# Performance work log

Measured on AMD Instinct MI355X. Metric: run time of the kernel, lower is better.

## Reference

```python
import jax, jax.numpy as jnp
import numpy as np

N_HEADS = 8
HEAD_DIM = 64  # d_model // n_heads = 512 // 8


def setup_inputs() -> dict:
    key = jax.random.key(0)
    kq, kk, kv, km = jax.random.split(key, 4)
    B, C, H, L, D = 8, 4, N_HEADS, 512, HEAD_DIM
    q = jax.random.normal(kq, (B * C, H, L, D), dtype=jnp.float32)
    k = jax.random.normal(kk, (B * C, H, D, L), dtype=jnp.float32)  # pre-transposed, matmul(q, k) directly
    v = jax.random.normal(kv, (B * C, H, L, D), dtype=jnp.float32)
    attn_mask = jax.random.randint(km, (B, L, L), 0, 2).astype(bool)  # True = masked out
    return {"q": q, "k": k, "v": v, "attn_mask": attn_mask}


def reference(q, k, v, attn_mask):
    # q: [B*C, H, L, D]; k: [B*C, H, D, L]; v: [B*C, H, L, D]; attn_mask: [B, L, L] bool
    scale = jnp.asarray(HEAD_DIM ** (-0.5), dtype=q.dtype)
    scores = jnp.einsum('ghld,ghdm->ghlm', q, k) * scale  # [B*C, H, L, L]
    if attn_mask is not None:
        B = attn_mask.shape[0]
        C = q.shape[0] // B
        H, L = scores.shape[1], scores.shape[2]
        scores = scores.reshape(B, C, H, L, L)
        mask = attn_mask[:, None, None, :, :]  # broadcast over channels and heads
        scores = jnp.where(mask, -jnp.inf, scores)
        scores = scores.reshape(B * C, H, L, L)
    attn_weights = jax.nn.softmax(scores, axis=-1)  # dropout p=0.0 -> identity (eval)
    output = jnp.einsum('ghlm,ghmd->ghld', attn_weights, v)  # [B*C, H, L, D]
    return output
```

## Files before the change

kernel.cpp:

```cpp
#include <hip/hip_runtime.h>


typedef __attribute__((ext_vector_type(8)))  short bf16x8;
typedef __attribute__((ext_vector_type(16))) float f32x16;

union Frag4 { uint4 x; unsigned u[4]; bf16x8 v; };

__device__ __forceinline__ unsigned pk_bf16(float a, float b){
    unsigned ua = __builtin_bit_cast(unsigned, a) + 0x8000u;
    unsigned ub = __builtin_bit_cast(unsigned, b) + 0x8000u;
    return __builtin_amdgcn_perm(ub, ua, 0x07060302u);
}

__device__ __forceinline__ float fast_exp2(float x){
#if __has_builtin(__builtin_amdgcn_exp2f)
    return __builtin_amdgcn_exp2f(x);
#else
    return exp2f(x);
#endif
}

#define L2E 1.44269504088896f

__global__ __launch_bounds__(256, 4)
void attn_fused(const float* __restrict__ qg, const float* __restrict__ kg,
                const float* __restrict__ vg, const int* __restrict__ mg,
                float* __restrict__ og)
{
    __shared__ uint4 sKt4[64*8];
    __shared__ uint4 sVt4[64*8];

    const int t    = threadIdx.x;
    const int lane = t & 63;
    const int wv   = t >> 6;
    const int col  = lane & 31;
    const int h    = lane >> 5;

    const int bi   = blockIdx.x;
    const int s    = bi >> 3;
    const int head = (bi & 7)*32 + (s >> 2);
    const int qt   = s & 3;
    const int b    = bi & 7;

    const float* qh = qg + (size_t)head*32768;
    const float* kh = kg + (size_t)head*32768;
    const float* vh = vg + (size_t)head*32768;
    const int*   mb = mg + (size_t)b*262144 + (size_t)qt*128*512;
    float*       oh = og + (size_t)head*32768;

    Frag4 qf[4];
    {
        const int qrow = qt*128 + wv*32 + col;
        const float* qr = qh + qrow*64 + h*8;
        #pragma unroll
        for (int kt=0; kt<4; ++kt){
            float4 x0 = *(const float4*)(qr + kt*16);
            float4 x1 = *(const float4*)(qr + kt*16 + 4);
            qf[kt].u[0] = pk_bf16(x0.x*0.125f, x0.y*0.125f);
            qf[kt].u[1] = pk_bf16(x0.z*0.125f, x0.w*0.125f);
            qf[kt].u[2] = pk_bf16(x1.x*0.125f, x1.y*0.125f);
            qf[kt].u[3] = pk_bf16(x1.z*0.125f, x1.w*0.125f);
        }
    }

    f32x16 o0, o1;
    #pragma unroll
    for (int i=0;i<16;++i){ o0[i]=0.f; o1[i]=0.f; }
    float lsum = 0.f;

    for (int kb=0; kb<8; ++kb){
        __syncthreads();
        #pragma unroll
        for (int gi=0; gi<2; ++gi){
            const int g = wv + gi*4;
            const float* kp = kh + (size_t)(g*8)*512 + kb*64 + lane;
            float kv[8];
            #pragma unroll
            for (int dd=0; dd<8; ++dd) kv[dd] = kp[(size_t)dd*512];
            Frag4 w;
            w.u[0]=pk_bf16(kv[0],kv[1]); w.u[1]=pk_bf16(kv[2],kv[3]);
            w.u[2]=pk_bf16(kv[4],kv[5]); w.u[3]=pk_bf16(kv[6],kv[7]);
            sKt4[lane*8 + (g ^ (lane&7))] = w.x;
        }
        #pragma unroll
        for (int gi=0; gi<2; ++gi){
            const int g = wv + gi*4;
            const float* vp = vh + (size_t)(kb*64 + g*8)*64 + lane;
            float vv[8];
            #pragma unroll
            for (int mm=0; mm<8; ++mm) vv[mm] = vp[(size_t)mm*64];
            Frag4 w;
            w.u[0]=pk_bf16(vv[0],vv[1]); w.u[1]=pk_bf16(vv[2],vv[3]);
            w.u[2]=pk_bf16(vv[4],vv[5]); w.u[3]=pk_bf16(vv[6],vv[7]);
            sVt4[lane*8 + (g ^ (lane&7))] = w.x;
        }
        __syncthreads();

        const int qrl = wv*32 + col;
        const int* mrow = mb + (size_t)qrl*512 + kb*64;
        #pragma unroll
        for (int mt=0; mt<2; ++mt){
            f32x16 sc;
            #pragma unroll
            for (int i=0;i<16;++i) sc[i]=0.f;
            #pragma unroll
            for (int kt=0; kt<4; ++kt){
                const int r = mt*32 + col;
                Frag4 a; a.x = sKt4[r*8 + ((kt*2+h) ^ (r&7))];
                sc = __builtin_amdgcn_mfma_f32_32x32x16_bf16(a.v, qf[kt].v, sc, 0, 0, 0);
            }
            float p[16];
            #pragma unroll
            for (int rg=0; rg<4; ++rg){
                int4 mm = *(const int4*)(mrow + mt*32 + rg*8 + h*4);
                float e0 = mm.x ? 0.f : fast_exp2(sc[4*rg+0]*L2E);
                float e1 = mm.y ? 0.f : fast_exp2(sc[4*rg+1]*L2E);
                float e2 = mm.z ? 0.f : fast_exp2(sc[4*rg+2]*L2E);
                float e3 = mm.w ? 0.f : fast_exp2(sc[4*rg+3]*L2E);
                p[4*rg+0]=e0; p[4*rg+1]=e1; p[4*rg+2]=e2; p[4*rg+3]=e3;
                lsum += (e0+e1)+(e2+e3);
            }
            unsigned pp[8];
            #pragma unroll
            for (int r2=0; r2<8; ++r2) pp[r2] = pk_bf16(p[2*r2], p[2*r2+1]);

            #pragma unroll
            for (int c=0; c<2; ++c){
                unsigned keep0 = h ? pp[4*c+2] : pp[4*c+0];
                unsigned keep1 = h ? pp[4*c+3] : pp[4*c+1];
                unsigned give0 = h ? pp[4*c+0] : pp[4*c+2];
                unsigned give1 = h ? pp[4*c+1] : pp[4*c+3];
                unsigned got0 = (unsigned)__shfl_xor((int)give0, 32, 64);
                unsigned got1 = (unsigned)__shfl_xor((int)give1, 32, 64);
                Frag4 pa;
                pa.u[0] = h ? got0  : keep0;
                pa.u[1] = h ? got1  : keep1;
                pa.u[2] = h ? keep0 : got0;
                pa.u[3] = h ? keep1 : got1;
                const int gm = mt*4 + c*2 + h;
                Frag4 b0; b0.x = sVt4[col*8      + (gm ^ (col&7))];
                o0 = __builtin_amdgcn_mfma_f32_32x32x16_bf16(pa.v, b0.v, o0, 0, 0, 0);
                Frag4 b1; b1.x = sVt4[(32+col)*8 + (gm ^ ((32+col)&7))];
                o1 = __builtin_amdgcn_mfma_f32_32x32x16_bf16(pa.v, b1.v, o1, 0, 0, 0);
            }
        }
    }

    lsum += __shfl_xor(lsum, 32, 64);
    const float inv = 1.0f / lsum;
    float* ob = oh + (size_t)(qt*128 + wv*32)*64;
    #pragma unroll
    for (int r=0; r<16; ++r){
        const int qq = (r&3) + 8*(r>>2) + 4*h;
        const float iv = __shfl(inv, qq, 64);
        ob[(size_t)qq*64 + col]      = o0[r]*iv;
        ob[(size_t)qq*64 + 32 + col] = o1[r]*iv;
    }
}

extern "C" void kernel_launch(void* const* d_in, const int* in_sizes, int n_in,
                              void* d_out, int out_size, void* d_ws, size_t ws_size,
                              hipStream_t stream) {
    (void)in_sizes; (void)n_in; (void)d_ws; (void)ws_size; (void)out_size;
    const float* q = (const float*)d_in[0];
    const float* k = (const float*)d_in[1];
    const float* v = (const float*)d_in[2];
    const int*   m = (const int*)d_in[3];
    attn_fused<<<dim3(1024), dim3(256), 0, stream>>>(q, k, v, m, (float*)d_out);
}
```

Baseline: 174.9 us.

## Double-buffer K/V tiles in LDS and pre-pack attention mask to bitmask

Adds double-buffered shared memory for the K and V tiles. The next tile's global loads are issued before the current tile's MFMAs, and one barrier per iteration replaces two, to hide load latency. Separately, a pre-pass kernel packs the int32 mask into 64-bit ballot words in workspace, so the attention kernel reads 8 bytes per row-block instead of 256 bytes of ints. This costs an extra launch, doubles LDS use, and holds more registers for the prefetched values, which could reduce occupancy.

```diff
diff --git a/kernel.cpp b/kernel.cpp
--- a/kernel.cpp
+++ b/kernel.cpp
@@ -22,13 +22,29 @@
 
 #define L2E 1.44269504088896f
 
+__global__ __launch_bounds__(256)
+void pack_mask(const int* __restrict__ mg, unsigned long long* __restrict__ bits)
+{
+    const int t    = blockIdx.x*256 + threadIdx.x;
+    const int lane = t & 63;
+    const int w0   = t >> 6;
+    const int strd = (int)((gridDim.x*256) >> 6);
+    const int nW   = 8*512*8;
+    for (int i = w0; i < nW; i += strd){
+        int v = mg[(size_t)i*64 + lane];
+        unsigned long long m = __ballot(v != 0);
+        if (lane == 0) bits[i] = m;
+    }
+}
+
+template<int BITS>
 __global__ __launch_bounds__(256, 4)
 void attn_fused(const float* __restrict__ qg, const float* __restrict__ kg,
                 const float* __restrict__ vg, const int* __restrict__ mg,
-                float* __restrict__ og)
+                const unsigned* __restrict__ bits, float* __restrict__ og)
 {
-    __shared__ uint4 sKt4[64*8];
-    __shared__ uint4 sVt4[64*8];
+    __shared__ uint4 sKt4[2][64*8];
+    __shared__ uint4 sVt4[2][64*8];
 
     const int t    = threadIdx.x;
     const int lane = t & 63;
@@ -45,13 +61,18 @@
     const float* qh = qg + (size_t)head*32768;
     const float* kh = kg + (size_t)head*32768;
     const float* vh = vg + (size_t)head*32768;
-    const int*   mb = mg + (size_t)b*262144 + (size_t)qt*128*512;
     float*       oh = og + (size_t)head*32768;
+
+    const int qrl = wv*32 + col;
+    const int* mrow0 = BITS ? nullptr
+        : mg + (size_t)b*262144 + (size_t)(qt*128 + qrl)*512;
+    const unsigned* brow = BITS
+        ? bits + ((size_t)b*512 + qt*128 + qrl)*16
+        : nullptr;
 
     Frag4 qf[4];
     {
-        const int qrow = qt*128 + wv*32 + col;
-        const float* qr = qh + qrow*64 + h*8;
+        const float* qr = qh + (size_t)(qt*128 + qrl)*64 + h*8;
         #pragma unroll
         for (int kt=0; kt<4; ++kt){
             float4 x0 = *(const float4*)(qr + kt*16);
@@ -63,41 +84,68 @@
         }
     }
 
+    auto loadK = [&](int kb, float* kf){
+        #pragma unroll
+        for (int gi=0; gi<2; ++gi){
+            const float* kp = kh + (size_t)((wv + gi*4)*8)*512 + kb*64 + lane;
+            #pragma unroll
+            for (int dd=0; dd<8; ++dd) kf[gi*8+dd] = kp[(size_t)dd*512];
+        }
+    };
+    auto loadV = [&](int kb, float* vf){
+        #pragma unroll
+        for (int gi=0; gi<2; ++gi){
+            const float* vp = vh + (size_t)(kb*64 + (wv + gi*4)*8)*64 + lane;
+            #pragma unroll
+            for (int mm=0; mm<8; ++mm) vf[gi*8+mm] = vp[(size_t)mm*64];
+        }
+    };
+    auto writeK = [&](int buf, const float* kf){
+        #pragma unroll
+        for (int gi=0; gi<2; ++gi){
+            const int g = wv + gi*4;
+            Frag4 w;
+            w.u[0]=pk_bf16(kf[gi*8+0],kf[gi*8+1]);
+            w.u[1]=pk_bf16(kf[gi*8+2],kf[gi*8+3]);
+            w.u[2]=pk_bf16(kf[gi*8+4],kf[gi*8+5]);
+            w.u[3]=pk_bf16(kf[gi*8+6],kf[gi*8+7]);
+            sKt4[buf][lane*8 + (g ^ (lane&7))] = w.x;
+        }
+    };
+    auto writeV = [&](int buf, const float* vf){
+        #pragma unroll
+        for (int gi=0; gi<2; ++gi){
+            const int g = wv + gi*4;
+            Frag4 w;
+            w.u[0]=pk_bf16(vf[gi*8+0],vf[gi*8+1]);
+            w.u[1]=pk_bf16(vf[gi*8+2],vf[gi*8+3]);
+            w.u[2]=pk_bf16(vf[gi*8+4],vf[gi*8+5]);
+            w.u[3]=pk_bf16(vf[gi*8+6],vf[gi*8+7]);
+            sVt4[buf][lane*8 + (g ^ (lane&7))] = w.x;
+        }
+    };
+
     f32x16 o0, o1;
     #pragma unroll
     for (int i=0;i<16;++i){ o0[i]=0.f; o1[i]=0.f; }
     float lsum = 0.f;
 
+    {
+        float kf[16], vf[16];
+        loadK(0, kf); loadV(0, vf);
+        writeK(0, kf); writeV(0, vf);
+    }
+    __syncthreads();
+
     for (int kb=0; kb<8; ++kb){
-        __syncthreads();
-        #pragma unroll
-        for (int gi=0; gi<2; ++gi){
-            const int g = wv + gi*4;
-            const float* kp = kh + (size_t)(g*8)*512 + kb*64 + lane;
-            float kv[8];
-            #pragma unroll
-            for (int dd=0; dd<8; ++dd) kv[dd] = kp[(size_t)dd*512];
-            Frag4 w;
-            w.u[0]=pk_bf16(kv[0],kv[1]); w.u[1]=pk_bf16(kv[2],kv[3]);
-            w.u[2]=pk_bf16(kv[4],kv[5]); w.u[3]=pk_bf16(kv[6],kv[7]);
-            sKt4[lane*8 + (g ^ (lane&7))] = w.x;
-        }
-        #pragma unroll
-        for (int gi=0; gi<2; ++gi){
-            const int g = wv + gi*4;
-            const float* vp = vh + (size_t)(kb*64 + g*8)*64 + lane;
-            float vv[8];
-            #pragma unroll
-            for (int mm=0; mm<8; ++mm) vv[mm] = vp[(size_t)mm*64];
-            Frag4 w;
-            w.u[0]=pk_bf16(vv[0],vv[1]); w.u[1]=pk_bf16(vv[2],vv[3]);
-            w.u[2]=pk_bf16(vv[4],vv[5]); w.u[3]=pk_bf16(vv[6],vv[7]);
-            sVt4[lane*8 + (g ^ (lane&7))] = w.x;
-        }
-        __syncthreads();
-
-        const int qrl = wv*32 + col;
-        const int* mrow = mb + (size_t)qrl*512 + kb*64;
+        const int cur = kb & 1;
+
+        float kn[16], vn[16];
+        if (kb < 7){ loadK(kb+1, kn); loadV(kb+1, vn); }
+
+        uint2 mbv;
+        if constexpr (BITS) mbv = *(const uint2*)(brow + kb*2);
+
         #pragma unroll
         for (int mt=0; mt<2; ++mt){
             f32x16 sc;
@@ -106,19 +154,34 @@
             #pragma unroll
             for (int kt=0; kt<4; ++kt){
                 const int r = mt*32 + col;
-                Frag4 a; a.x = sKt4[r*8 + ((kt*2+h) ^ (r&7))];
+                Frag4 a; a.x = sKt4[cur][r*8 + ((kt*2+h) ^ (r&7))];
                 sc = __builtin_amdgcn_mfma_f32_32x32x16_bf16(a.v, qf[kt].v, sc, 0, 0, 0);
             }
             float p[16];
-            #pragma unroll
-            for (int rg=0; rg<4; ++rg){
-                int4 mm = *(const int4*)(mrow + mt*32 + rg*8 + h*4);
-                float e0 = mm.x ? 0.f : fast_exp2(sc[4*rg+0]*L2E);
-                float e1 = mm.y ? 0.f : fast_exp2(sc[4*rg+1]*L2E);
-                float e2 = mm.z ? 0.f : fast_exp2(sc[4*rg+2]*L2E);
-                float e3 = mm.w ? 0.f : fast_exp2(sc[4*rg+3]*L2E);
-                p[4*rg+0]=e0; p[4*rg+1]=e1; p[4*rg+2]=e2; p[4*rg+3]=e3;
-                lsum += (e0+e1)+(e2+e3);
+            if constexpr (BITS){
+                const unsigned mword = mt ? mbv.y : mbv.x;
+                #pragma unroll
+                for (int rg=0; rg<4; ++rg){
+                    const unsigned mw = mword >> (rg*8 + h*4);
+                    float e0 = (mw & 1u) ? 0.f : fast_exp2(sc[4*rg+0]*L2E);
+                    float e1 = (mw & 2u) ? 0.f : fast_exp2(sc[4*rg+1]*L2E);
+                    float e2 = (mw & 4u) ? 0.f : fast_exp2(sc[4*rg+2]*L2E);
+                    float e3 = (mw & 8u) ? 0.f : fast_exp2(sc[4*rg+3]*L2E);
+                    p[4*rg+0]=e0; p[4*rg+1]=e1; p[4*rg+2]=e2; p[4*rg+3]=e3;
+                    lsum += (e0+e1)+(e2+e3);
+                }
+            } else {
+                const int* mrow = mrow0 + kb*64;
+                #pragma unroll
+                for (int rg=0; rg<4; ++rg){
+                    int4 mm = *(const int4*)(mrow + mt*32 + rg*8 + h*4);
+                    float e0 = mm.x ? 0.f : fast_exp2(sc[4*rg+0]*L2E);
+                    float e1 = mm.y ? 0.f : fast_exp2(sc[4*rg+1]*L2E);
+                    float e2 = mm.z ? 0.f : fast_exp2(sc[4*rg+2]*L2E);
+                    float e3 = mm.w ? 0.f : fast_exp2(sc[4*rg+3]*L2E);
+                    p[4*rg+0]=e0; p[4*rg+1]=e1; p[4*rg+2]=e2; p[4*rg+3]=e3;
+                    lsum += (e0+e1)+(e2+e3);
+                }
             }
             unsigned pp[8];
             #pragma unroll
@@ -138,11 +201,16 @@
                 pa.u[2] = h ? keep0 : got0;
                 pa.u[3] = h ? keep1 : got1;
                 const int gm = mt*4 + c*2 + h;
-                Frag4 b0; b0.x = sVt4[col*8      + (gm ^ (col&7))];
+                Frag4 b0; b0.x = sVt4[cur][col*8      + (gm ^ (col&7))];
                 o0 = __builtin_amdgcn_mfma_f32_32x32x16_bf16(pa.v, b0.v, o0, 0, 0, 0);
-                Frag4 b1; b1.x = sVt4[(32+col)*8 + (gm ^ ((32+col)&7))];
+                Frag4 b1; b1.x = sVt4[cur][(32+col)*8 + (gm ^ ((32+col)&7))];
                 o1 = __builtin_amdgcn_mfma_f32_32x32x16_bf16(pa.v, b1.v, o1, 0, 0, 0);
             }
+        }
+
+        if (kb < 7){
+            writeK(cur^1, kn); writeV(cur^1, vn);
+            __syncthreads();
         }
     }
 
@@ -161,10 +229,18 @@
 extern "C" void kernel_launch(void* const* d_in, const int* in_sizes, int n_in,
                               void* d_out, int out_size, void* d_ws, size_t ws_size,
                               hipStream_t stream) {
-    (void)in_sizes; (void)n_in; (void)d_ws; (void)ws_size; (void)out_size;
+    (void)in_sizes; (void)n_in; (void)out_size;
     const float* q = (const float*)d_in[0];
     const float* k = (const float*)d_in[1];
     const float* v = (const float*)d_in[2];
     const int*   m = (const int*)d_in[3];
-    attn_fused<<<dim3(1024), dim3(256), 0, stream>>>(q, k, v, m, (float*)d_out);
-}
+    const size_t BITS_BYTES = (size_t)8*512*64;
+    if (d_ws && ws_size >= BITS_BYTES){
+        pack_mask<<<dim3(1024), dim3(256), 0, stream>>>(m, (unsigned long long*)d_ws);
+        attn_fused<1><<<dim3(1024), dim3(256), 0, stream>>>(
+            q, k, v, m, (const unsigned*)d_ws, (float*)d_out);
+    } else {
+        attn_fused<0><<<dim3(1024), dim3(256), 0, stream>>>(
+            q, k, v, m, nullptr, (float*)d_out);
+    }
+}
```

Measured after the change: 198.0 us. +13.2%, slower.

## Pre-pack attention mask into bitmask with a separate kernel

Applied to the files above, without the earlier changes.

Adds a pre-pass kernel that ballots the int32 mask into 64-bit words in the workspace. The attention kernel then reads two 32-bit words per 64-key block instead of 64 int32 values per row, which cuts mask traffic across the 32 heads that share each batch mask. It costs an extra launch plus a full read of the mask each call. The old path is kept as a fallback when no workspace is available.

```diff
diff --git a/kernel.cpp b/kernel.cpp
--- a/kernel.cpp
+++ b/kernel.cpp
@@ -22,10 +22,26 @@
 
 #define L2E 1.44269504088896f
 
+__global__ __launch_bounds__(256)
+void pack_mask(const int* __restrict__ mg, unsigned long long* __restrict__ bits)
+{
+    const int t    = blockIdx.x*256 + threadIdx.x;
+    const int lane = t & 63;
+    const int w0   = t >> 6;
+    const int strd = (int)((gridDim.x*256) >> 6);
+    const int nW   = 8*512*8;
+    for (int i = w0; i < nW; i += strd){
+        int v = mg[(size_t)i*64 + lane];
+        unsigned long long m = __ballot(v != 0);
+        if (lane == 0) bits[i] = m;
+    }
+}
+
+template<int BITS>
 __global__ __launch_bounds__(256, 4)
 void attn_fused(const float* __restrict__ qg, const float* __restrict__ kg,
                 const float* __restrict__ vg, const int* __restrict__ mg,
-                float* __restrict__ og)
+                const unsigned* __restrict__ bits, float* __restrict__ og)
 {
     __shared__ uint4 sKt4[64*8];
     __shared__ uint4 sVt4[64*8];
@@ -45,13 +61,18 @@
     const float* qh = qg + (size_t)head*32768;
     const float* kh = kg + (size_t)head*32768;
     const float* vh = vg + (size_t)head*32768;
-    const int*   mb = mg + (size_t)b*262144 + (size_t)qt*128*512;
     float*       oh = og + (size_t)head*32768;
+
+    const int qrl = wv*32 + col;
+    const int* mrow0 = BITS ? nullptr
+        : mg + (size_t)b*262144 + (size_t)(qt*128 + qrl)*512;
+    const unsigned* brow = BITS
+        ? bits + ((size_t)b*512 + qt*128 + qrl)*16
+        : nullptr;
 
     Frag4 qf[4];
     {
-        const int qrow = qt*128 + wv*32 + col;
-        const float* qr = qh + qrow*64 + h*8;
+        const float* qr = qh + (size_t)(qt*128 + qrl)*64 + h*8;
         #pragma unroll
         for (int kt=0; kt<4; ++kt){
             float4 x0 = *(const float4*)(qr + kt*16);
@@ -70,6 +91,10 @@
 
     for (int kb=0; kb<8; ++kb){
         __syncthreads();
+
+        uint2 mbv;
+        if constexpr (BITS) mbv = *(const uint2*)(brow + kb*2);
+
         #pragma unroll
         for (int gi=0; gi<2; ++gi){
             const int g = wv + gi*4;
@@ -96,8 +121,6 @@
         }
         __syncthreads();
 
-        const int qrl = wv*32 + col;
-        const int* mrow = mb + (size_t)qrl*512 + kb*64;
         #pragma unroll
         for (int mt=0; mt<2; ++mt){
             f32x16 sc;
@@ -110,15 +133,30 @@
                 sc = __builtin_amdgcn_mfma_f32_32x32x16_bf16(a.v, qf[kt].v, sc, 0, 0, 0);
             }
             float p[16];
-            #pragma unroll
-            for (int rg=0; rg<4; ++rg){
-                int4 mm = *(const int4*)(mrow + mt*32 + rg*8 + h*4);
-                float e0 = mm.x ? 0.f : fast_exp2(sc[4*rg+0]*L2E);
-                float e1 = mm.y ? 0.f : fast_exp2(sc[4*rg+1]*L2E);
-                float e2 = mm.z ? 0.f : fast_exp2(sc[4*rg+2]*L2E);
-                float e3 = mm.w ? 0.f : fast_exp2(sc[4*rg+3]*L2E);
-                p[4*rg+0]=e0; p[4*rg+1]=e1; p[4*rg+2]=e2; p[4*rg+3]=e3;
-                lsum += (e0+e1)+(e2+e3);
+            if constexpr (BITS){
+                const unsigned mword = mt ? mbv.y : mbv.x;
+                #pragma unroll
+                for (int rg=0; rg<4; ++rg){
+                    const unsigned mw = mword >> (rg*8 + h*4);
+                    float e0 = (mw & 1u) ? 0.f : fast_exp2(sc[4*rg+0]*L2E);
+                    float e1 = (mw & 2u) ? 0.f : fast_exp2(sc[4*rg+1]*L2E);
+                    float e2 = (mw & 4u) ? 0.f : fast_exp2(sc[4*rg+2]*L2E);
+                    float e3 = (mw & 8u) ? 0.f : fast_exp2(sc[4*rg+3]*L2E);
+                    p[4*rg+0]=e0; p[4*rg+1]=e1; p[4*rg+2]=e2; p[4*rg+3]=e3;
+                    lsum += (e0+e1)+(e2+e3);
+                }
+            } else {
+                const int* mrow = mrow0 + kb*64;
+                #pragma unroll
+                for (int rg=0; rg<4; ++rg){
+                    int4 mm = *(const int4*)(mrow + mt*32 + rg*8 + h*4);
+                    float e0 = mm.x ? 0.f : fast_exp2(sc[4*rg+0]*L2E);
+                    float e1 = mm.y ? 0.f : fast_exp2(sc[4*rg+1]*L2E);
+                    float e2 = mm.z ? 0.f : fast_exp2(sc[4*rg+2]*L2E);
+                    float e3 = mm.w ? 0.f : fast_exp2(sc[4*rg+3]*L2E);
+                    p[4*rg+0]=e0; p[4*rg+1]=e1; p[4*rg+2]=e2; p[4*rg+3]=e3;
+                    lsum += (e0+e1)+(e2+e3);
+                }
             }
             unsigned pp[8];
             #pragma unroll
@@ -161,10 +199,18 @@
 extern "C" void kernel_launch(void* const* d_in, const int* in_sizes, int n_in,
                               void* d_out, int out_size, void* d_ws, size_t ws_size,
                               hipStream_t stream) {
-    (void)in_sizes; (void)n_in; (void)d_ws; (void)ws_size; (void)out_size;
+    (void)in_sizes; (void)n_in; (void)out_size;
     const float* q = (const float*)d_in[0];
     const float* k = (const float*)d_in[1];
     const float* v = (const float*)d_in[2];
     const int*   m = (const int*)d_in[3];
-    attn_fused<<<dim3(1024), dim3(256), 0, stream>>>(q, k, v, m, (float*)d_out);
-}
+    const size_t BITS_BYTES = (size_t)8*512*64;
+    if (d_ws && ws_size >= BITS_BYTES){
+        pack_mask<<<dim3(1024), dim3(256), 0, stream>>>(m, (unsigned long long*)d_ws);
+        attn_fused<1><<<dim3(1024), dim3(256), 0, stream>>>(
+            q, k, v, m, (const unsigned*)d_ws, (float*)d_out);
+    } else {
+        attn_fused<0><<<dim3(1024), dim3(256), 0, stream>>>(
+            q, k, v, m, nullptr, (float*)d_out);
+    }
+}
```

Result: faster. 169.2 us (-3.3%).
